# Optimization experiments

Hardware: AMD Instinct MI355X
Metric: run time of the kernel (lower is better)

## Reference

```python
import jax, jax.numpy as jnp
import numpy as np

TOP_K = 2
N_TOKENS = 8192
D_IN = 2048
HIDDEN = 2048
N_EXPERTS = 8


def setup_inputs() -> dict:
    key = jax.random.key(0)
    ks = jax.random.split(key, 3)
    # 0.001 stddev matches RandomNormal(mean=0, stddev=0.001) initializers
    x = jax.random.normal(ks[0], (N_TOKENS, D_IN), dtype=jnp.float32)
    Wg = jax.random.normal(ks[1], (D_IN, N_EXPERTS), dtype=jnp.float32) * 0.001
    bg = jnp.zeros((N_EXPERTS,), dtype=jnp.float32)
    We = jax.random.normal(ks[2], (N_EXPERTS, D_IN, HIDDEN), dtype=jnp.float32) * 0.001
    be = jnp.zeros((N_EXPERTS, HIDDEN), dtype=jnp.float32)
    return {"x": x, "Wg": Wg, "bg": bg, "We": We, "be": be}


def reference(x, Wg, bg, We, be):
    # Gating: dense -> softmax over experts
    gating = jax.nn.softmax(x @ Wg + bg, axis=-1)          # [N, E]
    top_w, top_i = jax.lax.top_k(gating, TOP_K)            # [N, K] each
    # Dense all-expert compute (as in the original: every expert runs on every token)
    expert_out = jnp.einsum('nd,edh->neh', x, We) + be      # [N, E, H]
    # Gather the top-k expert outputs per token and combine with gating weights
    sel = jnp.take_along_axis(expert_out, top_i[:, :, None], axis=1)  # [N, K, H]
    combined = jnp.sum(sel * top_w[:, :, None], axis=1)    # [N, H]
    return combined
```

## Files before the change

### kernel.cpp

```cpp
#include <hip/hip_runtime.h>
#include <hip/hip_bf16.h>

#define N_TOKENS 8192
#define D_IN     2048
#define HIDDEN   2048
#define N_EXP    8
#define CAP      N_TOKENS
#define GATE_BLOCKS 2048
#define TPOSE_BLOCKS (N_EXP * 32 * 32)

typedef __bf16 bf16x8 __attribute__((ext_vector_type(8)));
typedef float  f32x4  __attribute__((ext_vector_type(4)));

#define OFF_CNT   0
#define OFF_TOK   4096
#define OFF_W     266240
#define OFF_XBF   1048576
#define OFF_WET   34603008
#define OFF_P1    101711872ull
#define WS_NEED   (OFF_P1 + (size_t)N_TOKENS * HIDDEN * 4)

__device__ __forceinline__ unsigned short f2bf(float f) {
  unsigned int u = __builtin_bit_cast(unsigned int, f);
  u += 0x7fffu + ((u >> 16) & 1u);
  return (unsigned short)(u >> 16);
}

__device__ __forceinline__ void g2l16(const void* g, void* l) {
  __builtin_amdgcn_global_load_lds(
      (__attribute__((address_space(1))) void*)g,
      (__attribute__((address_space(3))) void*)l, 16, 0, 0);
}

union PrepSM {
  float tile[64][68];
  struct {
    int   lcnt[8];
    int   base[8];
    int   ltok[8][8];
    float lw[8][8];
  } g;
};

__global__ __launch_bounds__(256) void prep_kernel(
    const float* __restrict__ x, const float* __restrict__ Wg,
    const float* __restrict__ bg, const float* __restrict__ We,
    unsigned short* __restrict__ xbf, unsigned short* __restrict__ wet,
    int* __restrict__ cnt, int* __restrict__ btok, float* __restrict__ bw)
{
  __shared__ PrepSM sm;
  const int tid = threadIdx.x;

  if (blockIdx.x >= GATE_BLOCKS) {
    const int id = blockIdx.x - GATE_BLOCKS;
    const int e  = id >> 10;
    const int rem = id & 1023;
    const int d0 = (rem >> 5) << 6;
    const int h0 = (rem & 31) << 6;
    const int r  = tid >> 2;
    const int g  = tid & 3;

    const float* src = We + ((size_t)e * D_IN + d0 + r) * HIDDEN + h0 + g * 16;
#pragma unroll
    for (int i = 0; i < 4; ++i)
      *(float4*)&sm.tile[r][g * 16 + i * 4] = *(const float4*)(src + i * 4);
    __syncthreads();

    union { unsigned short s[16]; uint4 q[2]; } u;
#pragma unroll
    for (int i = 0; i < 16; ++i) u.s[i] = f2bf(sm.tile[g * 16 + i][r]);
    uint4* dst = (uint4*)(wet + ((size_t)e * HIDDEN + h0 + r) * D_IN + d0 + g * 16);
    dst[0] = u.q[0];
    dst[1] = u.q[1];
    return;
  }

  const int lane = tid & 63;
  const int wid  = tid >> 6;
  if (tid < 8) sm.g.lcnt[tid] = 0;
  __syncthreads();

  {
    const int n = blockIdx.x * 4 + wid;
    const float* xr = x + (size_t)n * D_IN;
    unsigned short* xbr = xbf + (size_t)n * D_IN;

#pragma unroll
    for (int c = 0; c < 8; ++c) {
      const int d = c * 256 + lane * 4;
      float4 xv = *(const float4*)(xr + d);
      uint2 pk;
      pk.x = (unsigned int)f2bf(xv.x) | ((unsigned int)f2bf(xv.y) << 16);
      pk.y = (unsigned int)f2bf(xv.z) | ((unsigned int)f2bf(xv.w) << 16);
      *(uint2*)(xbr + d) = pk;
    }

    float acc[8];
#pragma unroll
    for (int e = 0; e < 8; ++e) acc[e] = 0.f;
#pragma unroll 4
    for (int c = 0; c < 32; ++c) {
      const int d = c * 64 + lane;
      const float xv = xr[d];
      const float4 g0 = *(const float4*)(Wg + (size_t)d * 8);
      const float4 g1 = *(const float4*)(Wg + (size_t)d * 8 + 4);
      acc[0] += xv * g0.x; acc[1] += xv * g0.y;
      acc[2] += xv * g0.z; acc[3] += xv * g0.w;
      acc[4] += xv * g1.x; acc[5] += xv * g1.y;
      acc[6] += xv * g1.z; acc[7] += xv * g1.w;
    }
#pragma unroll
    for (int e = 0; e < 8; ++e) {
      float v = acc[e];
      v += __shfl_down(v, 32); v += __shfl_down(v, 16); v += __shfl_down(v, 8);
      v += __shfl_down(v, 4);  v += __shfl_down(v, 2);  v += __shfl_down(v, 1);
      acc[e] = v;
    }

    if (lane == 0) {
      float lg[8], p[8];
      float mx = -1e30f;
#pragma unroll
      for (int e = 0; e < 8; ++e) { lg[e] = acc[e] + bg[e]; mx = fmaxf(mx, lg[e]); }
      float s = 0.f;
#pragma unroll
      for (int e = 0; e < 8; ++e) { p[e] = expf(lg[e] - mx); s += p[e]; }
      const float inv = 1.f / s;
      int e1 = 0;
#pragma unroll
      for (int e = 1; e < 8; ++e) if (lg[e] > lg[e1]) e1 = e;
      int e2 = (e1 == 0) ? 1 : 0;
#pragma unroll
      for (int e = 0; e < 8; ++e) if (e != e1 && lg[e] > lg[e2]) e2 = e;

      const int s1 = atomicAdd(&sm.g.lcnt[e1], 1);
      sm.g.ltok[e1][s1] = n;              sm.g.lw[e1][s1] = p[e1] * inv;
      const int s2 = atomicAdd(&sm.g.lcnt[e2], 1);
      sm.g.ltok[e2][s2] = n | (1 << 13);  sm.g.lw[e2][s2] = p[e2] * inv;
    }
  }
  __syncthreads();

  if (tid < 8) sm.g.base[tid] = atomicAdd(&cnt[tid * 32], sm.g.lcnt[tid]);
  __syncthreads();

  const int e = tid >> 5, i = tid & 31;
  if (i < sm.g.lcnt[e]) {
    const int o = e * CAP + sm.g.base[e] + i;
    btok[o] = sm.g.ltok[e][i];
    bw[o]   = sm.g.lw[e][i];
  }
}

template <int SLOTTED>
__global__ __launch_bounds__(256, 4) void moe_gemm(
    const unsigned short* __restrict__ xbf, const unsigned short* __restrict__ wet,
    const float* __restrict__ be, const int* __restrict__ cnt,
    const int* __restrict__ btok, const float* __restrict__ bw,
    float* __restrict__ out, float* __restrict__ p1)
{
  const int flat = blockIdx.x + (blockIdx.y << 4) + (blockIdx.z << 10);
  const int swz  = ((flat & 7) << 10) + (flat >> 3);
  const int e    = swz >> 10;
  const int h0   = ((swz >> 6) & 15) << 7;
  const int m0   = (swz & 63) << 7;

  const int M = cnt[e * 32];
  if (m0 >= M) return;

  __shared__ __align__(16) unsigned short As[128 * 64];
  __shared__ __align__(16) unsigned short Bs[128 * 64];

  const int tid  = threadIdx.x;
  const int wid  = tid >> 6;
  const int lane = tid & 63;
  const int wm   = wid >> 1;
  const int wn   = wid & 1;

  const int* etok = btok + e * CAP;
  const float* ew = bw + e * CAP;

  const int kcs = (((lane & 7) ^ (lane >> 3)) * 8);

  size_t asrc[4], bsrc[4];
#pragma unroll
  for (int j = 0; j < 4; ++j) {
    const int c = wid * 4 + j;
    const int r = c * 8 + (lane >> 3);
    int ar = m0 + r;
    if (ar >= M) ar = m0;
    const int tok = etok[ar] & 8191;
    asrc[j] = (size_t)tok * D_IN + kcs;
    bsrc[j] = ((size_t)e * HIDDEN + h0 + r) * D_IN + kcs;
  }

  f32x4 acc[4][4];
#pragma unroll
  for (int i = 0; i < 4; ++i)
#pragma unroll
    for (int j = 0; j < 4; ++j) acc[i][j] = (f32x4){0.f, 0.f, 0.f, 0.f};

  for (int k0 = 0; k0 < D_IN; k0 += 64) {
    __syncthreads();
#pragma unroll
    for (int j = 0; j < 4; ++j)
      g2l16(xbf + asrc[j] + k0, &As[(wid * 4 + j) * 512]);
#pragma unroll
    for (int j = 0; j < 4; ++j)
      g2l16(wet + bsrc[j] + k0, &Bs[(wid * 4 + j) * 512]);
    __syncthreads();

#pragma unroll
    for (int kh = 0; kh < 2; ++kh) {
      bf16x8 af[4], bfr[4];
#pragma unroll
      for (int fm = 0; fm < 4; ++fm) {
        const int row = wm * 64 + fm * 16 + (lane & 15);
        const int kc  = kh * 4 + (lane >> 4);
        af[fm] = __builtin_bit_cast(bf16x8,
            *(const uint4*)(As + row * 64 + ((kc ^ (row & 7)) * 8)));
      }
#pragma unroll
      for (int fn = 0; fn < 4; ++fn) {
        const int row = wn * 64 + fn * 16 + (lane & 15);
        const int kc  = kh * 4 + (lane >> 4);
        bfr[fn] = __builtin_bit_cast(bf16x8,
            *(const uint4*)(Bs + row * 64 + ((kc ^ (row & 7)) * 8)));
      }
#pragma unroll
      for (int fm = 0; fm < 4; ++fm)
#pragma unroll
        for (int fn = 0; fn < 4; ++fn)
          acc[fm][fn] = __builtin_amdgcn_mfma_f32_16x16x32_bf16(
              af[fm], bfr[fn], acc[fm][fn], 0, 0, 0);
    }
  }

  float bias[4];
#pragma unroll
  for (int fn = 0; fn < 4; ++fn)
    bias[fn] = be[e * HIDDEN + h0 + wn * 64 + fn * 16 + (lane & 15)];

#pragma unroll
  for (int fm = 0; fm < 4; ++fm) {
    const int rbase = m0 + wm * 64 + fm * 16 + (lane >> 4) * 4;
#pragma unroll
    for (int reg = 0; reg < 4; ++reg) {
      const int r = rbase + reg;
      if (r < M) {
        const int tv  = etok[r];
        const int tok = tv & 8191;
        const float w = ew[r];
        if (SLOTTED) {
          float* dst = ((tv >> 13) ? p1 : out) +
                       (size_t)tok * HIDDEN + h0 + wn * 64 + (lane & 15);
#pragma unroll
          for (int fn = 0; fn < 4; ++fn)
            dst[fn * 16] = w * (acc[fm][fn][reg] + bias[fn]);
        } else {
          float* orow = out + (size_t)tok * HIDDEN + h0 + wn * 64 + (lane & 15);
#pragma unroll
          for (int fn = 0; fn < 4; ++fn)
            atomicAdd(orow + fn * 16, w * (acc[fm][fn][reg] + bias[fn]));
        }
      }
    }
  }
}

__global__ __launch_bounds__(256) void combine_kernel(
    float* __restrict__ out, const float* __restrict__ p1)
{
  const int stride = gridDim.x * 256;
  for (int i = blockIdx.x * 256 + threadIdx.x;
       i < N_TOKENS * HIDDEN / 4; i += stride) {
    float4 a = ((const float4*)out)[i];
    const float4 b = ((const float4*)p1)[i];
    a.x += b.x; a.y += b.y; a.z += b.z; a.w += b.w;
    ((float4*)out)[i] = a;
  }
}

extern "C" void kernel_launch(void* const* d_in, const int* in_sizes, int n_in,
                              void* d_out, int out_size, void* d_ws, size_t ws_size,
                              hipStream_t stream) {
  const float* x  = (const float*)d_in[0];
  const float* Wg = (const float*)d_in[1];
  const float* bg = (const float*)d_in[2];
  const float* We = (const float*)d_in[3];
  const float* be = (const float*)d_in[4];
  float* out = (float*)d_out;

  char* ws = (char*)d_ws;
  int*            cnt  = (int*)(ws + OFF_CNT);
  int*            btok = (int*)(ws + OFF_TOK);
  float*          bw   = (float*)(ws + OFF_W);
  unsigned short* xbf  = (unsigned short*)(ws + OFF_XBF);
  unsigned short* wet  = (unsigned short*)(ws + OFF_WET);
  float*          p1   = (float*)(ws + OFF_P1);

  const bool slotted = (ws_size >= WS_NEED);

  hipMemsetAsync(cnt, 0, 8 * 32 * sizeof(int), stream);
  if (!slotted)
    hipMemsetAsync(d_out, 0, (size_t)out_size * sizeof(float), stream);

  prep_kernel<<<GATE_BLOCKS + TPOSE_BLOCKS, 256, 0, stream>>>(
      x, Wg, bg, We, xbf, wet, cnt, btok, bw);

  if (slotted) {
    moe_gemm<1><<<dim3(HIDDEN / 128, N_TOKENS / 128, N_EXP), 256, 0, stream>>>(
        xbf, wet, be, cnt, btok, bw, out, p1);
    combine_kernel<<<2048, 256, 0, stream>>>(out, p1);
  } else {
    moe_gemm<0><<<dim3(HIDDEN / 128, N_TOKENS / 128, N_EXP), 256, 0, stream>>>(
        xbf, wet, be, cnt, btok, bw, out, p1);
  }
}
```

Baseline: 470.4 us.

## Double-buffer GEMM LDS tiles, split prep into transpose and gate kernels

The MoE GEMM now double-buffers its A/B shared tiles so global-to-LDS loads for the next K step are issued while MFMAs run on the current step, leaving one barrier per iteration. Launch bounds drop from 4 to 2 blocks per CU to fit the doubled LDS. The combined prep kernel is split into separate transpose and gate kernels. The gate kernel reuses the float4 x loads from the bf16 conversion for the gating dot product instead of re-reading x. Risks are lower occupancy and an extra kernel launch.

```diff
diff --git a/kernel.cpp b/kernel.cpp
--- a/kernel.cpp
+++ b/kernel.cpp
@@ -32,128 +32,124 @@
       (__attribute__((address_space(3))) void*)l, 16, 0, 0);
 }
 
-union PrepSM {
-  float tile[64][68];
-  struct {
-    int   lcnt[8];
-    int   base[8];
-    int   ltok[8][8];
-    float lw[8][8];
-  } g;
+__global__ __launch_bounds__(256) void tpose_kernel(
+    const float* __restrict__ We, unsigned short* __restrict__ wet)
+{
+  __shared__ float tile[64][68];
+  const int tid = threadIdx.x;
+  const int id  = blockIdx.x;
+  const int e   = id >> 10;
+  const int rem = id & 1023;
+  const int d0  = (rem >> 5) << 6;
+  const int h0  = (rem & 31) << 6;
+  const int r   = tid >> 2;
+  const int g   = tid & 3;
+
+  const float* src = We + ((size_t)e * D_IN + d0 + r) * HIDDEN + h0 + g * 16;
+#pragma unroll
+  for (int i = 0; i < 4; ++i)
+    *(float4*)&tile[r][g * 16 + i * 4] = *(const float4*)(src + i * 4);
+  __syncthreads();
+
+  union { unsigned short s[16]; uint4 q[2]; } u;
+#pragma unroll
+  for (int i = 0; i < 16; ++i) u.s[i] = f2bf(tile[g * 16 + i][r]);
+  uint4* dst = (uint4*)(wet + ((size_t)e * HIDDEN + h0 + r) * D_IN + d0 + g * 16);
+  dst[0] = u.q[0];
+  dst[1] = u.q[1];
+}
+
+struct GateSM {
+  int   lcnt[8];
+  int   base[8];
+  int   ltok[8][8];
+  float lw[8][8];
 };
 
-__global__ __launch_bounds__(256) void prep_kernel(
+__global__ __launch_bounds__(256) void gate_kernel(
     const float* __restrict__ x, const float* __restrict__ Wg,
-    const float* __restrict__ bg, const float* __restrict__ We,
-    unsigned short* __restrict__ xbf, unsigned short* __restrict__ wet,
+    const float* __restrict__ bg, unsigned short* __restrict__ xbf,
     int* __restrict__ cnt, int* __restrict__ btok, float* __restrict__ bw)
 {
-  __shared__ PrepSM sm;
-  const int tid = threadIdx.x;
-
-  if (blockIdx.x >= GATE_BLOCKS) {
-    const int id = blockIdx.x - GATE_BLOCKS;
-    const int e  = id >> 10;
-    const int rem = id & 1023;
-    const int d0 = (rem >> 5) << 6;
-    const int h0 = (rem & 31) << 6;
-    const int r  = tid >> 2;
-    const int g  = tid & 3;
-
-    const float* src = We + ((size_t)e * D_IN + d0 + r) * HIDDEN + h0 + g * 16;
-#pragma unroll
-    for (int i = 0; i < 4; ++i)
-      *(float4*)&sm.tile[r][g * 16 + i * 4] = *(const float4*)(src + i * 4);
-    __syncthreads();
-
-    union { unsigned short s[16]; uint4 q[2]; } u;
-#pragma unroll
-    for (int i = 0; i < 16; ++i) u.s[i] = f2bf(sm.tile[g * 16 + i][r]);
-    uint4* dst = (uint4*)(wet + ((size_t)e * HIDDEN + h0 + r) * D_IN + d0 + g * 16);
-    dst[0] = u.q[0];
-    dst[1] = u.q[1];
-    return;
-  }
-
+  __shared__ GateSM sm;
+  const int tid  = threadIdx.x;
   const int lane = tid & 63;
   const int wid  = tid >> 6;
-  if (tid < 8) sm.g.lcnt[tid] = 0;
-  __syncthreads();
-
-  {
-    const int n = blockIdx.x * 4 + wid;
-    const float* xr = x + (size_t)n * D_IN;
-    unsigned short* xbr = xbf + (size_t)n * D_IN;
-
-#pragma unroll
-    for (int c = 0; c < 8; ++c) {
-      const int d = c * 256 + lane * 4;
-      float4 xv = *(const float4*)(xr + d);
-      uint2 pk;
-      pk.x = (unsigned int)f2bf(xv.x) | ((unsigned int)f2bf(xv.y) << 16);
-      pk.y = (unsigned int)f2bf(xv.z) | ((unsigned int)f2bf(xv.w) << 16);
-      *(uint2*)(xbr + d) = pk;
+  if (tid < 8) sm.lcnt[tid] = 0;
+  __syncthreads();
+
+  const int n = blockIdx.x * 4 + wid;
+  const float* xr = x + (size_t)n * D_IN;
+  unsigned short* xbr = xbf + (size_t)n * D_IN;
+
+  float acc[8];
+#pragma unroll
+  for (int e = 0; e < 8; ++e) acc[e] = 0.f;
+
+#pragma unroll
+  for (int c = 0; c < 8; ++c) {
+    const int d = c * 256 + lane * 4;
+    const float4 xv = *(const float4*)(xr + d);
+    uint2 pk;
+    pk.x = (unsigned int)f2bf(xv.x) | ((unsigned int)f2bf(xv.y) << 16);
+    pk.y = (unsigned int)f2bf(xv.z) | ((unsigned int)f2bf(xv.w) << 16);
+    *(uint2*)(xbr + d) = pk;
+    const float xs[4] = {xv.x, xv.y, xv.z, xv.w};
+#pragma unroll
+    for (int j = 0; j < 4; ++j) {
+      const float4 g0 = *(const float4*)(Wg + (size_t)(d + j) * 8);
+      const float4 g1 = *(const float4*)(Wg + (size_t)(d + j) * 8 + 4);
+      acc[0] += xs[j] * g0.x; acc[1] += xs[j] * g0.y;
+      acc[2] += xs[j] * g0.z; acc[3] += xs[j] * g0.w;
+      acc[4] += xs[j] * g1.x; acc[5] += xs[j] * g1.y;
+      acc[6] += xs[j] * g1.z; acc[7] += xs[j] * g1.w;
     }
-
-    float acc[8];
-#pragma unroll
-    for (int e = 0; e < 8; ++e) acc[e] = 0.f;
-#pragma unroll 4
-    for (int c = 0; c < 32; ++c) {
-      const int d = c * 64 + lane;
-      const float xv = xr[d];
-      const float4 g0 = *(const float4*)(Wg + (size_t)d * 8);
-      const float4 g1 = *(const float4*)(Wg + (size_t)d * 8 + 4);
-      acc[0] += xv * g0.x; acc[1] += xv * g0.y;
-      acc[2] += xv * g0.z; acc[3] += xv * g0.w;
-      acc[4] += xv * g1.x; acc[5] += xv * g1.y;
-      acc[6] += xv * g1.z; acc[7] += xv * g1.w;
-    }
-#pragma unroll
-    for (int e = 0; e < 8; ++e) {
-      float v = acc[e];
-      v += __shfl_down(v, 32); v += __shfl_down(v, 16); v += __shfl_down(v, 8);
-      v += __shfl_down(v, 4);  v += __shfl_down(v, 2);  v += __shfl_down(v, 1);
-      acc[e] = v;
-    }
-
-    if (lane == 0) {
-      float lg[8], p[8];
-      float mx = -1e30f;
-#pragma unroll
-      for (int e = 0; e < 8; ++e) { lg[e] = acc[e] + bg[e]; mx = fmaxf(mx, lg[e]); }
-      float s = 0.f;
-#pragma unroll
-      for (int e = 0; e < 8; ++e) { p[e] = expf(lg[e] - mx); s += p[e]; }
-      const float inv = 1.f / s;
-      int e1 = 0;
-#pragma unroll
-      for (int e = 1; e < 8; ++e) if (lg[e] > lg[e1]) e1 = e;
-      int e2 = (e1 == 0) ? 1 : 0;
-#pragma unroll
-      for (int e = 0; e < 8; ++e) if (e != e1 && lg[e] > lg[e2]) e2 = e;
-
-      const int s1 = atomicAdd(&sm.g.lcnt[e1], 1);
-      sm.g.ltok[e1][s1] = n;              sm.g.lw[e1][s1] = p[e1] * inv;
-      const int s2 = atomicAdd(&sm.g.lcnt[e2], 1);
-      sm.g.ltok[e2][s2] = n | (1 << 13);  sm.g.lw[e2][s2] = p[e2] * inv;
-    }
-  }
-  __syncthreads();
-
-  if (tid < 8) sm.g.base[tid] = atomicAdd(&cnt[tid * 32], sm.g.lcnt[tid]);
+  }
+
+#pragma unroll
+  for (int e = 0; e < 8; ++e) {
+    float v = acc[e];
+    v += __shfl_down(v, 32); v += __shfl_down(v, 16); v += __shfl_down(v, 8);
+    v += __shfl_down(v, 4);  v += __shfl_down(v, 2);  v += __shfl_down(v, 1);
+    acc[e] = v;
+  }
+
+  if (lane == 0) {
+    float lg[8], p[8];
+    float mx = -1e30f;
+#pragma unroll
+    for (int e = 0; e < 8; ++e) { lg[e] = acc[e] + bg[e]; mx = fmaxf(mx, lg[e]); }
+    float s = 0.f;
+#pragma unroll
+    for (int e = 0; e < 8; ++e) { p[e] = expf(lg[e] - mx); s += p[e]; }
+    const float inv = 1.f / s;
+    int e1 = 0;
+#pragma unroll
+    for (int e = 1; e < 8; ++e) if (lg[e] > lg[e1]) e1 = e;
+    int e2 = (e1 == 0) ? 1 : 0;
+#pragma unroll
+    for (int e = 0; e < 8; ++e) if (e != e1 && lg[e] > lg[e2]) e2 = e;
+
+    const int s1 = atomicAdd(&sm.lcnt[e1], 1);
+    sm.ltok[e1][s1] = n;              sm.lw[e1][s1] = p[e1] * inv;
+    const int s2 = atomicAdd(&sm.lcnt[e2], 1);
+    sm.ltok[e2][s2] = n | (1 << 13);  sm.lw[e2][s2] = p[e2] * inv;
+  }
+  __syncthreads();
+
+  if (tid < 8) sm.base[tid] = atomicAdd(&cnt[tid * 32], sm.lcnt[tid]);
   __syncthreads();
 
   const int e = tid >> 5, i = tid & 31;
-  if (i < sm.g.lcnt[e]) {
-    const int o = e * CAP + sm.g.base[e] + i;
-    btok[o] = sm.g.ltok[e][i];
-    bw[o]   = sm.g.lw[e][i];
+  if (i < sm.lcnt[e]) {
+    const int o = e * CAP + sm.base[e] + i;
+    btok[o] = sm.ltok[e][i];
+    bw[o]   = sm.lw[e][i];
   }
 }
 
 template <int SLOTTED>
-__global__ __launch_bounds__(256, 4) void moe_gemm(
+__global__ __launch_bounds__(256, 2) void moe_gemm(
     const unsigned short* __restrict__ xbf, const unsigned short* __restrict__ wet,
     const float* __restrict__ be, const int* __restrict__ cnt,
     const int* __restrict__ btok, const float* __restrict__ bw,
@@ -168,8 +164,8 @@
   const int M = cnt[e * 32];
   if (m0 >= M) return;
 
-  __shared__ __align__(16) unsigned short As[128 * 64];
-  __shared__ __align__(16) unsigned short Bs[128 * 64];
+  __shared__ __align__(16) unsigned short As[2][128 * 64];
+  __shared__ __align__(16) unsigned short Bs[2][128 * 64];
 
   const int tid  = threadIdx.x;
   const int wid  = tid >> 6;
@@ -200,16 +196,27 @@
 #pragma unroll
     for (int j = 0; j < 4; ++j) acc[i][j] = (f32x4){0.f, 0.f, 0.f, 0.f};
 
-  for (int k0 = 0; k0 < D_IN; k0 += 64) {
-    __syncthreads();
-#pragma unroll
-    for (int j = 0; j < 4; ++j)
-      g2l16(xbf + asrc[j] + k0, &As[(wid * 4 + j) * 512]);
-#pragma unroll
-    for (int j = 0; j < 4; ++j)
-      g2l16(wet + bsrc[j] + k0, &Bs[(wid * 4 + j) * 512]);
-    __syncthreads();
-
+#define STAGE(b_, k_) {                                                        \
+    _Pragma("unroll")                                                          \
+    for (int j = 0; j < 4; ++j)                                                \
+      g2l16(xbf + asrc[j] + (k_), &As[b_][(wid * 4 + j) * 512]);               \
+    _Pragma("unroll")                                                          \
+    for (int j = 0; j < 4; ++j)                                                \
+      g2l16(wet + bsrc[j] + (k_), &Bs[b_][(wid * 4 + j) * 512]); }
+
+  STAGE(0, 0);
+  __syncthreads();
+
+  int cur = 0;
+#pragma unroll 1
+  for (int t = 0; t < D_IN / 64; ++t) {
+    const int kn = (t + 1) * 64;
+    if (kn < D_IN) {
+      if (cur) STAGE(0, kn) else STAGE(1, kn);
+    }
+
+    const unsigned short* Ab = &As[cur][0];
+    const unsigned short* Bb = &Bs[cur][0];
 #pragma unroll
     for (int kh = 0; kh < 2; ++kh) {
       bf16x8 af[4], bfr[4];
@@ -218,14 +225,14 @@
         const int row = wm * 64 + fm * 16 + (lane & 15);
         const int kc  = kh * 4 + (lane >> 4);
         af[fm] = __builtin_bit_cast(bf16x8,
-            *(const uint4*)(As + row * 64 + ((kc ^ (row & 7)) * 8)));
+            *(const uint4*)(Ab + row * 64 + ((kc ^ (row & 7)) * 8)));
       }
 #pragma unroll
       for (int fn = 0; fn < 4; ++fn) {
         const int row = wn * 64 + fn * 16 + (lane & 15);
         const int kc  = kh * 4 + (lane >> 4);
         bfr[fn] = __builtin_bit_cast(bf16x8,
-            *(const uint4*)(Bs + row * 64 + ((kc ^ (row & 7)) * 8)));
+            *(const uint4*)(Bb + row * 64 + ((kc ^ (row & 7)) * 8)));
       }
 #pragma unroll
       for (int fm = 0; fm < 4; ++fm)
@@ -234,7 +241,11 @@
           acc[fm][fn] = __builtin_amdgcn_mfma_f32_16x16x32_bf16(
               af[fm], bfr[fn], acc[fm][fn], 0, 0, 0);
     }
-  }
+
+    __syncthreads();
+    cur ^= 1;
+  }
+#undef STAGE
 
   float bias[4];
 #pragma unroll
@@ -305,8 +316,8 @@
   if (!slotted)
     hipMemsetAsync(d_out, 0, (size_t)out_size * sizeof(float), stream);
 
-  prep_kernel<<<GATE_BLOCKS + TPOSE_BLOCKS, 256, 0, stream>>>(
-      x, Wg, bg, We, xbf, wet, cnt, btok, bw);
+  tpose_kernel<<<TPOSE_BLOCKS, 256, 0, stream>>>(We, wet);
+  gate_kernel<<<GATE_BLOCKS, 256, 0, stream>>>(x, Wg, bg, xbf, cnt, btok, bw);
 
   if (slotted) {
     moe_gemm<1><<<dim3(HIDDEN / 128, N_TOKENS / 128, N_EXP), 256, 0, stream>>>(
```

Measured after the change: 544.1 us. +15.7%, slower.
